# Kernel optimization log

Hardware: AMD Instinct MI355X
Metric: run time of the kernel (lower is better)

The kernel has to match this reference:

```python
import jax, jax.numpy as jnp
import numpy as np

DIM = 64        # feature size per vector
CODES = 512     # codebook size (called d_model in the torch module)
DECAY = 0.99
EPS = 1e-5


def setup_inputs() -> dict:
    key = jax.random.key(0)
    k1, k2 = jax.random.split(key)
    x = jax.random.normal(k1, (64, 64, 64, 64), dtype=jnp.float32)
    embedding = jax.random.normal(k2, (DIM, CODES), dtype=jnp.float32)
    N = jnp.zeros((CODES,), dtype=jnp.float32)
    M = embedding.copy()  # torch module initializes M as embedding.clone()
    return {"x": x, "embedding": embedding, "N": N, "M": M}


def reference(x, embedding, N, M):
    # flatten tokens: [T, DIM]
    flatten = x.reshape(-1, DIM)
    # squared L2 distance to every code: [T, CODES]
    distance = (jnp.sum(flatten * flatten, axis=1, keepdims=True)
                - 2.0 * flatten @ embedding
                + jnp.sum(embedding * embedding, axis=0, keepdims=True))
    max_index = jnp.argmin(distance, axis=1)          # (-distance).max(1) == argmin
    indices = max_index.reshape(x.shape[:-1])
    # gather codes: embedding.T is [CODES, DIM]
    quantize = jnp.take(embedding.T, max_index, axis=0).reshape(x.shape)

    # EMA codebook update (training=True). Avoid materializing onehot:
    # ni = onehot.sum(0); eofx = flatten.T @ onehot  -> segment sums over codes.
    ni = jax.ops.segment_sum(jnp.ones_like(max_index, dtype=jnp.float32),
                             max_index, num_segments=CODES)          # [CODES]
    eofx = jax.ops.segment_sum(flatten, max_index, num_segments=CODES).T  # [DIM, CODES]
    N_new = N * DECAY + (1.0 - DECAY) * ni
    M_new = M * DECAY + (1.0 - DECAY) * eofx
    n = jnp.sum(N_new)
    N_smoothed = (N_new + EPS) / (n + CODES * EPS) * n
    embedding_new = M_new / N_smoothed

    quant_loss = jnp.mean((jax.lax.stop_gradient(x) - quantize) ** 2)
    commitment_loss = jnp.mean((jax.lax.stop_gradient(quantize) - x) ** 2)
    quantize_st = x + jax.lax.stop_gradient(quantize - x)  # straight-through
    return (quantize_st, quant_loss, indices, commitment_loss,
            embedding_new, N_new, M_new)
```

## Files before the change

### kernel.cpp

```cpp
#include <hip/hip_runtime.h>
#include <hip/hip_bf16.h>
#include <math.h>

#define DIM 64
#define CODES 512
#define TOKENS 262144
#define XELEMS 16777216

#define DECAYF 0.99f
#define OMDECAY 0.01f
#define EPSF 1e-5f

#define WS_CNORM 0
#define WS_NI    512
#define WS_EOFX  1024
#define WS_LOSS  33792
#define WS_ET    33808
#define WS_IMG   66576
#define WS_PART  99344
#define PART_STRIDE 33280
#define NPART 512

#define OFF_Q    0
#define OFF_QL   16777216
#define OFF_IDX  16777217
#define OFF_CL   17039361
#define OFF_ENEW 17039362
#define OFF_NNEW 17072130
#define OFF_MNEW 17072642

typedef __attribute__((ext_vector_type(8))) short bf16x8;
typedef __attribute__((ext_vector_type(4))) float f32x4;

static __device__ inline void split_bf(float v, short& hi, short& lo) {
  unsigned int b = __float_as_uint(v);
  unsigned int hb = b & 0xffff0000u;
  float lof = v - __uint_as_float(hb);
  hi = (short)(b >> 16);
  lo = (short)(__float_as_uint(lof) >> 16);
}
static __device__ inline float bf2f(short s) {
  unsigned int u = ((unsigned int)(unsigned short)s) << 16;
  return __uint_as_float(u);
}

__global__ __launch_bounds__(256) void vq_prep(const float* __restrict__ emb,
                                               float* __restrict__ ws) {
  int c = blockIdx.x * 256 + threadIdx.x;
  unsigned short* img = (unsigned short*)(ws + WS_IMG);
  float* eT = ws + WS_ET;
  int cc = c >> 4;
  int n = c & 15;
  float cn = 0.f;
#pragma unroll
  for (int d0 = 0; d0 < DIM; d0 += 4) {
    float v[4];
#pragma unroll
    for (int u = 0; u < 4; ++u) {
      v[u] = emb[(d0 + u) * CODES + c];
      cn = fmaf(v[u], v[u], cn);
    }
    *(float4*)(eT + (size_t)c * DIM + d0) = make_float4(v[0], v[1], v[2], v[3]);
    int kh = d0 >> 5, kk = d0 & 31, qd = kk >> 3, j0 = kk & 7;
    int lane = qd * 16 + n;
    short hi[4], lo[4];
#pragma unroll
    for (int u = 0; u < 4; ++u) split_bf(v[u], hi[u], lo[u]);
    int base = cc * 2048 + kh * 1024 + lane * 8 + j0;
    *(ushort4*)(img + base) =
        make_ushort4((unsigned short)hi[0], (unsigned short)hi[1],
                     (unsigned short)hi[2], (unsigned short)hi[3]);
    *(ushort4*)(img + base + 512) =
        make_ushort4((unsigned short)lo[0], (unsigned short)lo[1],
                     (unsigned short)lo[2], (unsigned short)lo[3]);
  }
  ws[WS_CNORM + c] = cn;
}

__global__ __launch_bounds__(512, 2) void vq_fused(
    const float* __restrict__ x, const float* __restrict__ ws,
    float* __restrict__ loss_sum, float* __restrict__ q_out,
    float* __restrict__ idx_out, float* __restrict__ part_base, int aflush,
    float* __restrict__ ws_acc) {
  __shared__ __align__(16) unsigned char smem[135424];
  unsigned short* bimg = (unsigned short*)smem;
  float* cn_l = (float*)(smem + 131072);
  int* win_l = (int*)(smem + 133376);
  float* lds_n = (float*)smem;
  float* lds_e = (float*)(smem + 2048);

  const float* eT = ws + WS_ET;

  {
    const float4* src = (const float4*)(ws + WS_IMG);
    float4* dst = (float4*)bimg;
    for (int i = threadIdx.x; i < 8192; i += 512) dst[i] = src[i];
    for (int i = threadIdx.x; i < CODES; i += 512) cn_l[i] = ws[WS_CNORM + i];
  }
  __syncthreads();

  const int lane = threadIdx.x & 63;
  const int wave = threadIdx.x >> 6;
  const int n = lane & 15;
  const int quad = lane >> 4;
  const int t0 = blockIdx.x * 512 + wave * 64;

  bf16x8 ah[4][2], al[4][2];
#pragma unroll
  for (int tile = 0; tile < 4; ++tile) {
    const float* xr = x + (size_t)(t0 + tile * 16 + n) * DIM + quad * 8;
#pragma unroll
    for (int kh = 0; kh < 2; ++kh) {
      float4 v0 = *(const float4*)(xr + kh * 32);
      float4 v1v = *(const float4*)(xr + kh * 32 + 4);
      float f[8] = {v0.x, v0.y, v0.z, v0.w, v1v.x, v1v.y, v1v.z, v1v.w};
#pragma unroll
      for (int j = 0; j < 8; ++j) {
        short hi, lo;
        split_bf(-2.f * f[j], hi, lo);
        ah[tile][kh][j] = hi;
        al[tile][kh][j] = lo;
      }
    }
  }

  const float INITP = __uint_as_float((__float_as_uint(1e30f) & 0xFFFFFE00u) | 511u);
  float v1[4][4], v2[4][4];
#pragma unroll
  for (int tile = 0; tile < 4; ++tile)
#pragma unroll
    for (int r = 0; r < 4; ++r) {
      v1[tile][r] = INITP;
      v2[tile][r] = INITP;
    }

  for (int cc = 0; cc < 32; ++cc) {
    const unsigned short* bp = bimg + cc * 2048;
    bf16x8 bh0 = *(const bf16x8*)(bp + lane * 8);
    bf16x8 bl0 = *(const bf16x8*)(bp + 512 + lane * 8);
    bf16x8 bh1 = *(const bf16x8*)(bp + 1024 + lane * 8);
    bf16x8 bl1 = *(const bf16x8*)(bp + 1536 + lane * 8);
    float cnv = cn_l[cc * 16 + n];
    unsigned int cid = (unsigned int)(cc * 16 + n);
#pragma unroll
    for (int tile = 0; tile < 4; ++tile) {
      f32x4 acc = {0.f, 0.f, 0.f, 0.f};
      acc = __builtin_amdgcn_mfma_f32_16x16x32_bf16(ah[tile][0], bh0, acc, 0, 0, 0);
      acc = __builtin_amdgcn_mfma_f32_16x16x32_bf16(al[tile][0], bh0, acc, 0, 0, 0);
      acc = __builtin_amdgcn_mfma_f32_16x16x32_bf16(ah[tile][0], bl0, acc, 0, 0, 0);
      acc = __builtin_amdgcn_mfma_f32_16x16x32_bf16(ah[tile][1], bh1, acc, 0, 0, 0);
      acc = __builtin_amdgcn_mfma_f32_16x16x32_bf16(al[tile][1], bh1, acc, 0, 0, 0);
      acc = __builtin_amdgcn_mfma_f32_16x16x32_bf16(ah[tile][1], bl1, acc, 0, 0, 0);
#pragma unroll
      for (int r = 0; r < 4; ++r) {
        float s = acc[r] + cnv;
        float sp = __uint_as_float((__float_as_uint(s) & 0xFFFFFE00u) | cid);
        float o1 = v1[tile][r];
        v2[tile][r] = __builtin_amdgcn_fmed3f(sp, o1, v2[tile][r]);
        v1[tile][r] = fminf(sp, o1);
      }
    }
  }

#pragma unroll
  for (int m = 1; m < 16; m <<= 1) {
#pragma unroll
    for (int tile = 0; tile < 4; ++tile)
#pragma unroll
      for (int r = 0; r < 4; ++r) {
        float o1 = __shfl_xor(v1[tile][r], m, 16);
        float o2 = __shfl_xor(v2[tile][r], m, 16);
        float a = v1[tile][r];
        v1[tile][r] = fminf(a, o1);
        v2[tile][r] = fminf(fminf(v2[tile][r], o2), fmaxf(a, o1));
      }
  }

  float loss = 0.f;
#pragma unroll
  for (int tile = 0; tile < 4; ++tile) {
#pragma unroll
    for (int r = 0; r < 4; ++r) {
      int t = t0 + tile * 16 + quad * 4 + r;
      int c1 = (int)(__float_as_uint(v1[tile][r]) & 511u);
      int c2 = (int)(__float_as_uint(v2[tile][r]) & 511u);
      float4 xv = *(const float4*)(x + (size_t)t * DIM + n * 4);
      float4 e1 = *(const float4*)(eT + (size_t)c1 * DIM + n * 4);
      float4 e2 = *(const float4*)(eT + (size_t)c2 * DIM + n * 4);
      float p1 = xv.x * e1.x;
      p1 = fmaf(xv.y, e1.y, p1);
      p1 = fmaf(xv.z, e1.z, p1);
      p1 = fmaf(xv.w, e1.w, p1);
      float p2 = xv.x * e2.x;
      p2 = fmaf(xv.y, e2.y, p2);
      p2 = fmaf(xv.z, e2.z, p2);
      p2 = fmaf(xv.w, e2.w, p2);
#pragma unroll
      for (int m = 1; m < 16; m <<= 1) {
        p1 += __shfl_xor(p1, m, 16);
        p2 += __shfl_xor(p2, m, 16);
      }
      float d1 = fmaf(-2.f, p1, cn_l[c1]);
      float d2 = fmaf(-2.f, p2, cn_l[c2]);
      bool take2 = (d2 < d1) || (d2 == d1 && c2 < c1);
      int w = take2 ? c2 : c1;
      float4 q = take2 ? e2 : e1;
      *(float4*)(q_out + (size_t)t * DIM + n * 4) = q;
      float u0 = xv.x - q.x, u1 = xv.y - q.y;
      float u2 = xv.z - q.z, u3 = xv.w - q.w;
      loss = fmaf(u0, u0, loss);
      loss = fmaf(u1, u1, loss);
      loss = fmaf(u2, u2, loss);
      loss = fmaf(u3, u3, loss);
      if (n == 0) {
        idx_out[t] = (float)w;
        win_l[wave * 64 + tile * 16 + quad * 4 + r] = w;
      }
    }
  }
#pragma unroll
  for (int off = 32; off > 0; off >>= 1) loss += __shfl_down(loss, off, 64);
  if (lane == 0) atomicAdd(loss_sum, loss);

  __syncthreads();
  {
    float4 z = make_float4(0.f, 0.f, 0.f, 0.f);
    float4* zp = (float4*)smem;
    for (int i = threadIdx.x; i < 133376 / 16; i += 512) zp[i] = z;
  }
  __syncthreads();

#pragma unroll
  for (int tile = 0; tile < 4; ++tile) {
    int wbi = win_l[wave * 64 + tile * 16 + n];
    if (quad == 0) atomicAdd(&lds_n[wbi], 1.0f);
#pragma unroll
    for (int kh = 0; kh < 2; ++kh) {
#pragma unroll
      for (int j = 0; j < 8; ++j) {
        float xk = -0.5f * (bf2f(ah[tile][kh][j]) + bf2f(al[tile][kh][j]));
        int k = kh * 32 + quad * 8 + j;
        atomicAdd(&lds_e[k * 513 + wbi], xk);
      }
    }
  }
  __syncthreads();

  if (aflush) {
    for (int i = threadIdx.x; i < CODES; i += 512) {
      float v = lds_n[i];
      if (v != 0.f) atomicAdd(&ws_acc[WS_NI + i], v);
    }
    for (int i = threadIdx.x; i < DIM * CODES; i += 512) {
      int k = i >> 9, c = i & 511;
      float v = lds_e[k * 513 + c];
      if (v != 0.f) atomicAdd(&ws_acc[WS_EOFX + i], v);
    }
  } else {
    float* dest = part_base + (size_t)blockIdx.x * PART_STRIDE;
    for (int i = threadIdx.x; i < CODES; i += 512) dest[i] = lds_n[i];
    for (int i = threadIdx.x; i < DIM * CODES; i += 512) {
      int k = i >> 9, c = i & 511;
      dest[CODES + i] = lds_e[k * 513 + c];
    }
  }
}

__global__ __launch_bounds__(256) void vq_reduce(const float* __restrict__ part,
                                                 float* __restrict__ ws, int P) {
  int i = blockIdx.x * 256 + threadIdx.x;
  if (i >= PART_STRIDE) return;
  float a0 = 0.f, a1 = 0.f, a2 = 0.f, a3 = 0.f;
  int p = 0;
  for (; p + 3 < P; p += 4) {
    a0 += part[(size_t)(p + 0) * PART_STRIDE + i];
    a1 += part[(size_t)(p + 1) * PART_STRIDE + i];
    a2 += part[(size_t)(p + 2) * PART_STRIDE + i];
    a3 += part[(size_t)(p + 3) * PART_STRIDE + i];
  }
  for (; p < P; ++p) a0 += part[(size_t)p * PART_STRIDE + i];
  ws[WS_NI + i] = (a0 + a1) + (a2 + a3);
}

__global__ __launch_bounds__(512) void vq_final(const float* __restrict__ Nin,
                                                const float* __restrict__ Min,
                                                const float* __restrict__ ws,
                                                float* __restrict__ out) {
  __shared__ float red[512];
  int c = threadIdx.x;
  int d = blockIdx.x;
  float niv = ws[WS_NI + c];
  float Nn = Nin[c] * DECAYF + OMDECAY * niv;
  red[c] = Nn;
  __syncthreads();
#pragma unroll
  for (int s = 256; s > 0; s >>= 1) {
    if (c < s) red[c] += red[c + s];
    __syncthreads();
  }
  float nsum = red[0];
  float Nsm = (Nn + EPSF) / (nsum + (float)CODES * EPSF) * nsum;
  float m = Min[d * CODES + c] * DECAYF + OMDECAY * ws[WS_EOFX + d * CODES + c];
  out[OFF_MNEW + d * CODES + c] = m;
  out[OFF_ENEW + d * CODES + c] = m / Nsm;
  if (d == 0) {
    out[OFF_NNEW + c] = Nn;
    if (c == 0) {
      float l = ws[WS_LOSS] / (float)XELEMS;
      out[OFF_QL] = l;
      out[OFF_CL] = l;
    }
  }
}

extern "C" void kernel_launch(void* const* d_in, const int* in_sizes, int n_in,
                              void* d_out, int out_size, void* d_ws, size_t ws_size,
                              hipStream_t stream) {
  const float* x = (const float*)d_in[0];
  const float* emb = (const float*)d_in[1];
  const float* Nin = (const float*)d_in[2];
  const float* Min = (const float*)d_in[3];
  float* out = (float*)d_out;
  float* ws = (float*)d_ws;

  size_t avail = ws_size / 4;
  int aflush = (avail < (size_t)WS_PART + (size_t)NPART * PART_STRIDE) ? 1 : 0;

  hipMemsetAsync(ws + WS_NI, 0, (size_t)(WS_ET - WS_NI) * sizeof(float), stream);

  vq_prep<<<2, 256, 0, stream>>>(emb, ws);

  vq_fused<<<TOKENS / 512, 512, 0, stream>>>(
      x, ws, ws + WS_LOSS, out + OFF_Q, out + OFF_IDX, ws + WS_PART, aflush, ws);

  if (!aflush) {
    vq_reduce<<<(PART_STRIDE + 255) / 256, 256, 0, stream>>>(ws + WS_PART, ws,
                                                             NPART);
  }

  vq_final<<<DIM, 512, 0, stream>>>(Nin, Min, ws, out);
}
```

Before: 363.6 us.

## Read codebook from global/L2 with prefetch and halve LDS for higher occupancy

Removes the 128KB LDS copy of the split-bf16 codebook image. MFMA B operands are now read directly from global memory with a double-buffered register prefetch. Tokens are processed in two passes of two tiles each to cut register pressure, and the EOFX LDS accumulator is split into two 32-dim halves so LDS drops to about 70KB. Together these target 4 blocks per CU instead of 2. The EOFX scatter re-reads x from global instead of reconstructing it from bf16 split registers. The cost is an L2/global read of the codebook image for every block, plus an extra sync and flush pass.

After: 350.2 us. 3.7% less time.

```diff
diff --git a/kernel.cpp b/kernel.cpp
--- a/kernel.cpp
+++ b/kernel.cpp
@@ -39,10 +39,6 @@
   hi = (short)(b >> 16);
   lo = (short)(__float_as_uint(lof) >> 16);
 }
-static __device__ inline float bf2f(short s) {
-  unsigned int u = ((unsigned int)(unsigned short)s) << 16;
-  return __uint_as_float(u);
-}
 
 __global__ __launch_bounds__(256) void vq_prep(const float* __restrict__ emb,
                                                float* __restrict__ ws) {
@@ -77,24 +73,24 @@
   ws[WS_CNORM + c] = cn;
 }
 
-__global__ __launch_bounds__(512, 2) void vq_fused(
+__global__ __launch_bounds__(512, 4) void vq_fused(
     const float* __restrict__ x, const float* __restrict__ ws,
     float* __restrict__ loss_sum, float* __restrict__ q_out,
     float* __restrict__ idx_out, float* __restrict__ part_base, int aflush,
     float* __restrict__ ws_acc) {
-  __shared__ __align__(16) unsigned char smem[135424];
-  unsigned short* bimg = (unsigned short*)smem;
-  float* cn_l = (float*)(smem + 131072);
-  int* win_l = (int*)(smem + 133376);
-  float* lds_n = (float*)smem;
-  float* lds_e = (float*)(smem + 2048);
+  __shared__ __align__(16) unsigned char smem[71808];
+  float* lds_e = (float*)smem;
+  float* lds_n = (float*)(smem + 65664);
+  float* cn_l = (float*)(smem + 67712);
+  int* win_l = (int*)(smem + 69760);
 
   const float* eT = ws + WS_ET;
+  const unsigned short* gimg = (const unsigned short*)(ws + WS_IMG);
 
   {
-    const float4* src = (const float4*)(ws + WS_IMG);
-    float4* dst = (float4*)bimg;
-    for (int i = threadIdx.x; i < 8192; i += 512) dst[i] = src[i];
+    float4 z = make_float4(0.f, 0.f, 0.f, 0.f);
+    float4* zp = (float4*)smem;
+    for (int i = threadIdx.x; i < 67712 / 16; i += 512) zp[i] = z;
     for (int i = threadIdx.x; i < CODES; i += 512) cn_l[i] = ws[WS_CNORM + i];
   }
   __syncthreads();
@@ -105,164 +101,194 @@
   const int quad = lane >> 4;
   const int t0 = blockIdx.x * 512 + wave * 64;
 
-  bf16x8 ah[4][2], al[4][2];
-#pragma unroll
-  for (int tile = 0; tile < 4; ++tile) {
-    const float* xr = x + (size_t)(t0 + tile * 16 + n) * DIM + quad * 8;
-#pragma unroll
-    for (int kh = 0; kh < 2; ++kh) {
-      float4 v0 = *(const float4*)(xr + kh * 32);
-      float4 v1v = *(const float4*)(xr + kh * 32 + 4);
-      float f[8] = {v0.x, v0.y, v0.z, v0.w, v1v.x, v1v.y, v1v.z, v1v.w};
-#pragma unroll
-      for (int j = 0; j < 8; ++j) {
-        short hi, lo;
-        split_bf(-2.f * f[j], hi, lo);
-        ah[tile][kh][j] = hi;
-        al[tile][kh][j] = lo;
-      }
-    }
-  }
-
   const float INITP = __uint_as_float((__float_as_uint(1e30f) & 0xFFFFFE00u) | 511u);
-  float v1[4][4], v2[4][4];
-#pragma unroll
-  for (int tile = 0; tile < 4; ++tile)
-#pragma unroll
-    for (int r = 0; r < 4; ++r) {
-      v1[tile][r] = INITP;
-      v2[tile][r] = INITP;
-    }
-
-  for (int cc = 0; cc < 32; ++cc) {
-    const unsigned short* bp = bimg + cc * 2048;
-    bf16x8 bh0 = *(const bf16x8*)(bp + lane * 8);
-    bf16x8 bl0 = *(const bf16x8*)(bp + 512 + lane * 8);
-    bf16x8 bh1 = *(const bf16x8*)(bp + 1024 + lane * 8);
-    bf16x8 bl1 = *(const bf16x8*)(bp + 1536 + lane * 8);
-    float cnv = cn_l[cc * 16 + n];
-    unsigned int cid = (unsigned int)(cc * 16 + n);
-#pragma unroll
-    for (int tile = 0; tile < 4; ++tile) {
-      f32x4 acc = {0.f, 0.f, 0.f, 0.f};
-      acc = __builtin_amdgcn_mfma_f32_16x16x32_bf16(ah[tile][0], bh0, acc, 0, 0, 0);
-      acc = __builtin_amdgcn_mfma_f32_16x16x32_bf16(al[tile][0], bh0, acc, 0, 0, 0);
-      acc = __builtin_amdgcn_mfma_f32_16x16x32_bf16(ah[tile][0], bl0, acc, 0, 0, 0);
-      acc = __builtin_amdgcn_mfma_f32_16x16x32_bf16(ah[tile][1], bh1, acc, 0, 0, 0);
-      acc = __builtin_amdgcn_mfma_f32_16x16x32_bf16(al[tile][1], bh1, acc, 0, 0, 0);
-      acc = __builtin_amdgcn_mfma_f32_16x16x32_bf16(ah[tile][1], bl1, acc, 0, 0, 0);
+  float loss = 0.f;
+
+#pragma unroll 1
+  for (int pair = 0; pair < 2; ++pair) {
+    bf16x8 ah[2][2], al[2][2];
+#pragma unroll
+    for (int tile = 0; tile < 2; ++tile) {
+      const float* xr =
+          x + (size_t)(t0 + (pair * 2 + tile) * 16 + n) * DIM + quad * 8;
+#pragma unroll
+      for (int kh = 0; kh < 2; ++kh) {
+        float4 va = *(const float4*)(xr + kh * 32);
+        float4 vb = *(const float4*)(xr + kh * 32 + 4);
+        float f[8] = {va.x, va.y, va.z, va.w, vb.x, vb.y, vb.z, vb.w};
+#pragma unroll
+        for (int j = 0; j < 8; ++j) {
+          short hi, lo;
+          split_bf(-2.f * f[j], hi, lo);
+          ah[tile][kh][j] = hi;
+          al[tile][kh][j] = lo;
+        }
+      }
+    }
+
+    float v1[2][4], v2[2][4];
+#pragma unroll
+    for (int tile = 0; tile < 2; ++tile)
 #pragma unroll
       for (int r = 0; r < 4; ++r) {
-        float s = acc[r] + cnv;
-        float sp = __uint_as_float((__float_as_uint(s) & 0xFFFFFE00u) | cid);
-        float o1 = v1[tile][r];
-        v2[tile][r] = __builtin_amdgcn_fmed3f(sp, o1, v2[tile][r]);
-        v1[tile][r] = fminf(sp, o1);
-      }
-    }
-  }
-
-#pragma unroll
-  for (int m = 1; m < 16; m <<= 1) {
-#pragma unroll
-    for (int tile = 0; tile < 4; ++tile)
+        v1[tile][r] = INITP;
+        v2[tile][r] = INITP;
+      }
+
+    bf16x8 Pa0, Pa1, Pa2, Pa3, Pb0, Pb1, Pb2, Pb3;
+    {
+      const unsigned short* bq = gimg + lane * 8;
+      Pa0 = *(const bf16x8*)(bq);
+      Pa1 = *(const bf16x8*)(bq + 512);
+      Pa2 = *(const bf16x8*)(bq + 1024);
+      Pa3 = *(const bf16x8*)(bq + 1536);
+    }
+
+    auto ccbody = [&](int cc, const bf16x8& ch0, const bf16x8& cl0,
+                      const bf16x8& ch1, const bf16x8& cl1, bf16x8& nh0,
+                      bf16x8& nl0, bf16x8& nh1, bf16x8& nl1) {
+      const unsigned short* bq = gimg + ((cc + 1) & 31) * 2048 + lane * 8;
+      nh0 = *(const bf16x8*)(bq);
+      nl0 = *(const bf16x8*)(bq + 512);
+      nh1 = *(const bf16x8*)(bq + 1024);
+      nl1 = *(const bf16x8*)(bq + 1536);
+      float cnv = cn_l[cc * 16 + n];
+      unsigned int cid = (unsigned int)(cc * 16 + n);
+#pragma unroll
+      for (int tile = 0; tile < 2; ++tile) {
+        f32x4 acc = {0.f, 0.f, 0.f, 0.f};
+        acc = __builtin_amdgcn_mfma_f32_16x16x32_bf16(ah[tile][0], ch0, acc, 0, 0, 0);
+        acc = __builtin_amdgcn_mfma_f32_16x16x32_bf16(al[tile][0], ch0, acc, 0, 0, 0);
+        acc = __builtin_amdgcn_mfma_f32_16x16x32_bf16(ah[tile][0], cl0, acc, 0, 0, 0);
+        acc = __builtin_amdgcn_mfma_f32_16x16x32_bf16(ah[tile][1], ch1, acc, 0, 0, 0);
+        acc = __builtin_amdgcn_mfma_f32_16x16x32_bf16(al[tile][1], ch1, acc, 0, 0, 0);
+        acc = __builtin_amdgcn_mfma_f32_16x16x32_bf16(ah[tile][1], cl1, acc, 0, 0, 0);
+#pragma unroll
+        for (int r = 0; r < 4; ++r) {
+          float s = acc[r] + cnv;
+          float sp = __uint_as_float((__float_as_uint(s) & 0xFFFFFE00u) | cid);
+          float o1 = v1[tile][r];
+          v2[tile][r] = __builtin_amdgcn_fmed3f(sp, o1, v2[tile][r]);
+          v1[tile][r] = fminf(sp, o1);
+        }
+      }
+    };
+
+    for (int cc = 0; cc < 32; cc += 2) {
+      ccbody(cc, Pa0, Pa1, Pa2, Pa3, Pb0, Pb1, Pb2, Pb3);
+      ccbody(cc + 1, Pb0, Pb1, Pb2, Pb3, Pa0, Pa1, Pa2, Pa3);
+    }
+
+#pragma unroll
+    for (int m = 1; m < 16; m <<= 1) {
+#pragma unroll
+      for (int tile = 0; tile < 2; ++tile)
+#pragma unroll
+        for (int r = 0; r < 4; ++r) {
+          float o1 = __shfl_xor(v1[tile][r], m, 16);
+          float o2 = __shfl_xor(v2[tile][r], m, 16);
+          float a = v1[tile][r];
+          v1[tile][r] = fminf(a, o1);
+          v2[tile][r] = fminf(fminf(v2[tile][r], o2), fmaxf(a, o1));
+        }
+    }
+
+#pragma unroll
+    for (int tile = 0; tile < 2; ++tile) {
+      int tt = pair * 2 + tile;
 #pragma unroll
       for (int r = 0; r < 4; ++r) {
-        float o1 = __shfl_xor(v1[tile][r], m, 16);
-        float o2 = __shfl_xor(v2[tile][r], m, 16);
-        float a = v1[tile][r];
-        v1[tile][r] = fminf(a, o1);
-        v2[tile][r] = fminf(fminf(v2[tile][r], o2), fmaxf(a, o1));
-      }
-  }
-
-  float loss = 0.f;
-#pragma unroll
-  for (int tile = 0; tile < 4; ++tile) {
-#pragma unroll
-    for (int r = 0; r < 4; ++r) {
-      int t = t0 + tile * 16 + quad * 4 + r;
-      int c1 = (int)(__float_as_uint(v1[tile][r]) & 511u);
-      int c2 = (int)(__float_as_uint(v2[tile][r]) & 511u);
-      float4 xv = *(const float4*)(x + (size_t)t * DIM + n * 4);
-      float4 e1 = *(const float4*)(eT + (size_t)c1 * DIM + n * 4);
-      float4 e2 = *(const float4*)(eT + (size_t)c2 * DIM + n * 4);
-      float p1 = xv.x * e1.x;
-      p1 = fmaf(xv.y, e1.y, p1);
-      p1 = fmaf(xv.z, e1.z, p1);
-      p1 = fmaf(xv.w, e1.w, p1);
-      float p2 = xv.x * e2.x;
-      p2 = fmaf(xv.y, e2.y, p2);
-      p2 = fmaf(xv.z, e2.z, p2);
-      p2 = fmaf(xv.w, e2.w, p2);
-#pragma unroll
-      for (int m = 1; m < 16; m <<= 1) {
-        p1 += __shfl_xor(p1, m, 16);
-        p2 += __shfl_xor(p2, m, 16);
-      }
-      float d1 = fmaf(-2.f, p1, cn_l[c1]);
-      float d2 = fmaf(-2.f, p2, cn_l[c2]);
-      bool take2 = (d2 < d1) || (d2 == d1 && c2 < c1);
-      int w = take2 ? c2 : c1;
-      float4 q = take2 ? e2 : e1;
-      *(float4*)(q_out + (size_t)t * DIM + n * 4) = q;
-      float u0 = xv.x - q.x, u1 = xv.y - q.y;
-      float u2 = xv.z - q.z, u3 = xv.w - q.w;
-      loss = fmaf(u0, u0, loss);
-      loss = fmaf(u1, u1, loss);
-      loss = fmaf(u2, u2, loss);
-      loss = fmaf(u3, u3, loss);
-      if (n == 0) {
-        idx_out[t] = (float)w;
-        win_l[wave * 64 + tile * 16 + quad * 4 + r] = w;
-      }
-    }
-  }
+        int t = t0 + tt * 16 + quad * 4 + r;
+        int c1 = (int)(__float_as_uint(v1[tile][r]) & 511u);
+        int c2 = (int)(__float_as_uint(v2[tile][r]) & 511u);
+        float4 xv = *(const float4*)(x + (size_t)t * DIM + n * 4);
+        float4 e1 = *(const float4*)(eT + (size_t)c1 * DIM + n * 4);
+        float4 e2 = *(const float4*)(eT + (size_t)c2 * DIM + n * 4);
+        float p1 = xv.x * e1.x;
+        p1 = fmaf(xv.y, e1.y, p1);
+        p1 = fmaf(xv.z, e1.z, p1);
+        p1 = fmaf(xv.w, e1.w, p1);
+        float p2 = xv.x * e2.x;
+        p2 = fmaf(xv.y, e2.y, p2);
+        p2 = fmaf(xv.z, e2.z, p2);
+        p2 = fmaf(xv.w, e2.w, p2);
+#pragma unroll
+        for (int m = 1; m < 16; m <<= 1) {
+          p1 += __shfl_xor(p1, m, 16);
+          p2 += __shfl_xor(p2, m, 16);
+        }
+        float d1 = fmaf(-2.f, p1, cn_l[c1]);
+        float d2 = fmaf(-2.f, p2, cn_l[c2]);
+        bool take2 = (d2 < d1) || (d2 == d1 && c2 < c1);
+        int w = take2 ? c2 : c1;
+        float4 q = take2 ? e2 : e1;
+        *(float4*)(q_out + (size_t)t * DIM + n * 4) = q;
+        float u0 = xv.x - q.x, u1 = xv.y - q.y;
+        float u2 = xv.z - q.z, u3 = xv.w - q.w;
+        loss = fmaf(u0, u0, loss);
+        loss = fmaf(u1, u1, loss);
+        loss = fmaf(u2, u2, loss);
+        loss = fmaf(u3, u3, loss);
+        if (n == 0) {
+          idx_out[t] = (float)w;
+          win_l[wave * 64 + tt * 16 + quad * 4 + r] = w;
+        }
+      }
+    }
+  }
+
 #pragma unroll
   for (int off = 32; off > 0; off >>= 1) loss += __shfl_down(loss, off, 64);
   if (lane == 0) atomicAdd(loss_sum, loss);
 
   __syncthreads();
-  {
-    float4 z = make_float4(0.f, 0.f, 0.f, 0.f);
-    float4* zp = (float4*)smem;
-    for (int i = threadIdx.x; i < 133376 / 16; i += 512) zp[i] = z;
-  }
-  __syncthreads();
-
-#pragma unroll
-  for (int tile = 0; tile < 4; ++tile) {
-    int wbi = win_l[wave * 64 + tile * 16 + n];
-    if (quad == 0) atomicAdd(&lds_n[wbi], 1.0f);
-#pragma unroll
-    for (int kh = 0; kh < 2; ++kh) {
-#pragma unroll
-      for (int j = 0; j < 8; ++j) {
-        float xk = -0.5f * (bf2f(ah[tile][kh][j]) + bf2f(al[tile][kh][j]));
-        int k = kh * 32 + quad * 8 + j;
-        atomicAdd(&lds_e[k * 513 + wbi], xk);
-      }
-    }
-  }
-  __syncthreads();
-
-  if (aflush) {
-    for (int i = threadIdx.x; i < CODES; i += 512) {
-      float v = lds_n[i];
-      if (v != 0.f) atomicAdd(&ws_acc[WS_NI + i], v);
-    }
-    for (int i = threadIdx.x; i < DIM * CODES; i += 512) {
-      int k = i >> 9, c = i & 511;
-      float v = lds_e[k * 513 + c];
-      if (v != 0.f) atomicAdd(&ws_acc[WS_EOFX + i], v);
-    }
-  } else {
-    float* dest = part_base + (size_t)blockIdx.x * PART_STRIDE;
-    for (int i = threadIdx.x; i < CODES; i += 512) dest[i] = lds_n[i];
-    for (int i = threadIdx.x; i < DIM * CODES; i += 512) {
-      int k = i >> 9, c = i & 511;
-      dest[CODES + i] = lds_e[k * 513 + c];
-    }
+
+#pragma unroll 1
+  for (int kh = 0; kh < 2; ++kh) {
+#pragma unroll
+    for (int tile = 0; tile < 4; ++tile) {
+      int wbi = win_l[wave * 64 + tile * 16 + n];
+      if (kh == 0 && quad == 0) atomicAdd(&lds_n[wbi], 1.0f);
+      const float* xr =
+          x + (size_t)(t0 + tile * 16 + n) * DIM + kh * 32 + quad * 8;
+      float4 xa = *(const float4*)(xr);
+      float4 xb = *(const float4*)(xr + 4);
+      int k0 = quad * 8;
+      atomicAdd(&lds_e[(k0 + 0) * 513 + wbi], xa.x);
+      atomicAdd(&lds_e[(k0 + 1) * 513 + wbi], xa.y);
+      atomicAdd(&lds_e[(k0 + 2) * 513 + wbi], xa.z);
+      atomicAdd(&lds_e[(k0 + 3) * 513 + wbi], xa.w);
+      atomicAdd(&lds_e[(k0 + 4) * 513 + wbi], xb.x);
+      atomicAdd(&lds_e[(k0 + 5) * 513 + wbi], xb.y);
+      atomicAdd(&lds_e[(k0 + 6) * 513 + wbi], xb.z);
+      atomicAdd(&lds_e[(k0 + 7) * 513 + wbi], xb.w);
+    }
+    __syncthreads();
+    if (aflush) {
+      if (kh == 0) {
+        for (int i = threadIdx.x; i < CODES; i += 512) {
+          float v = lds_n[i];
+          if (v != 0.f) atomicAdd(&ws_acc[WS_NI + i], v);
+        }
+      }
+      for (int i = threadIdx.x; i < 32 * CODES; i += 512) {
+        int k = i >> 9, c = i & 511;
+        float v = lds_e[k * 513 + c];
+        if (v != 0.f) atomicAdd(&ws_acc[WS_EOFX + kh * 32 * CODES + i], v);
+        if (kh == 0) lds_e[k * 513 + c] = 0.f;
+      }
+    } else {
+      float* dest = part_base + (size_t)blockIdx.x * PART_STRIDE;
+      if (kh == 0) {
+        for (int i = threadIdx.x; i < CODES; i += 512) dest[i] = lds_n[i];
+      }
+      for (int i = threadIdx.x; i < 32 * CODES; i += 512) {
+        int k = i >> 9, c = i & 511;
+        dest[CODES + kh * 32 * CODES + i] = lds_e[k * 513 + c];
+        if (kh == 0) lds_e[k * 513 + c] = 0.f;
+      }
+    }
+    if (kh == 0) __syncthreads();
   }
 }
 
```
